# Optimization experiments

Measured on AMD Instinct MI355X. Metric: run time of the kernel, lower is better.

## Reference

```python
import jax, jax.numpy as jnp
import numpy as np

HEADS = 16
HEAD_DIM = 64
QUAD_C = 5.0   # 2quad: exp(x) ~ (x + c)^2
EPS = 1e-6


def setup_inputs() -> dict:
    key = jax.random.key(0)
    k1, k2, k3 = jax.random.split(key, 3)
    B, T, H = 2, 2048, 1024
    x = jax.random.normal(k1, (B, T, H), dtype=jnp.float32)
    # scaled init to keep pre-activation scores sane
    Wqkv = jax.random.normal(k2, (H, 3 * H), dtype=jnp.float32) * (H ** -0.5)
    Wo = jax.random.normal(k3, (H, H), dtype=jnp.float32) * (H ** -0.5)
    tau = jnp.full((HEADS,), 5.0, dtype=jnp.float32)
    return {"x": x, "Wqkv": Wqkv, "Wo": Wo, "tau": tau}


def reference(x, Wqkv, Wo, tau):
    B, T, C = x.shape
    h, d = HEADS, HEAD_DIM
    qkv = x @ Wqkv                                  # [B,T,3C]
    q, k, v = jnp.split(qkv, 3, axis=-1)
    q = q.reshape(B, T, h, d).transpose(0, 2, 1, 3)  # [B,h,T,d]
    k = k.reshape(B, T, h, d).transpose(0, 2, 1, 3)
    v = v.reshape(B, T, h, d).transpose(0, 2, 1, 3)
    # tau-scaled scores
    s = jnp.einsum("bhqd,bhkd->bhqk", q, k) / (jnp.sqrt(jnp.float32(d)) * tau[None, :, None, None])
    # 2quad attention: (s + c)^2 normalized over keys (non-softmax)
    e = jnp.square(s + QUAD_C)                       # [B,h,T,T], >=0
    w = e / (jnp.sum(e, axis=-1, keepdims=True) + EPS)
    out = jnp.einsum("bhqk,bhkd->bhqd", w, v)        # [B,h,T,d]
    out = out.transpose(0, 2, 1, 3).reshape(B, T, C)
    return out @ Wo
```

## Files before the change

kernel.cpp:

```cpp
#include <hip/hip_runtime.h>
#include <hip/hip_bf16.h>


typedef unsigned short ushort_t;
typedef __attribute__((ext_vector_type(8))) short short8;
typedef __attribute__((ext_vector_type(4))) float f32x4;
typedef __attribute__((ext_vector_type(16))) float f32x16;

#define B_      2
#define T_      2048
#define C_      1024
#define HEADS_  16
#define D_      64

union frag_u { unsigned u[4]; short8 s8; };

__device__ __forceinline__ ushort_t f2bf(float f) {
  __hip_bfloat16 h = __float2bfloat16(f);
  return *reinterpret_cast<ushort_t*>(&h);
}

__device__ __forceinline__ unsigned cvt_pk_bf16(float lo, float hi) {
  unsigned r;
  asm("v_cvt_pk_bf16_f32 %0, %1, %2" : "=v"(r) : "v"(lo), "v"(hi));
  return r;
}

__device__ __forceinline__ void permlane32_swap(unsigned &a, unsigned &b) {
  asm volatile("v_permlane32_swap_b32 %0, %1" : "+v"(a), "+v"(b));
}

__device__ __forceinline__ f32x16 zero16() {
  f32x16 z;
#pragma unroll
  for (int i = 0; i < 16; ++i) z[i] = 0.f;
  return z;
}

__global__ __launch_bounds__(256) void cast_x_kernel(const float* __restrict__ x,
                                                     ushort_t* __restrict__ xb) {
  int i = blockIdx.x * 256 + threadIdx.x;
  float4 f = ((const float4*)x)[i];
  ushort_t* o = xb + (size_t)i * 4;
  o[0] = f2bf(f.x); o[1] = f2bf(f.y); o[2] = f2bf(f.z); o[3] = f2bf(f.w);
}

__global__ __launch_bounds__(256) void transpose_cast_w(const float* __restrict__ in,
                                                        ushort_t* __restrict__ out,
                                                        int R, int Cc) {
  __shared__ float tile[64][65];
  int rb = blockIdx.y, cb = blockIdx.x;
  int c = threadIdx.x & 63;
  int r0 = threadIdx.x >> 6;
#pragma unroll
  for (int i = 0; i < 16; ++i) {
    int r = r0 + i * 4;
    tile[r][c] = in[(size_t)(rb * 64 + r) * Cc + cb * 64 + c];
  }
  __syncthreads();
#pragma unroll
  for (int i = 0; i < 16; ++i) {
    int r = r0 + i * 4;
    out[(size_t)(cb * 64 + r) * R + rb * 64 + c] = f2bf(tile[c][r]);
  }
}

__global__ __launch_bounds__(256) void transpose_v_kernel(const ushort_t* __restrict__ v,
                                                          ushort_t* __restrict__ vT) {
  __shared__ ushort_t tile[64][72];
  int bh = blockIdx.y, tb = blockIdx.x;
  int c = threadIdx.x & 63;
  int r0 = threadIdx.x >> 6;
#pragma unroll
  for (int i = 0; i < 16; ++i) {
    int r = r0 + i * 4;
    tile[r][c] = v[((size_t)bh * T_ + tb * 64 + r) * D_ + c];
  }
  __syncthreads();
#pragma unroll
  for (int i = 0; i < 16; ++i) {
    int r = r0 + i * 4;
    vT[((size_t)bh * D_ + r) * T_ + tb * 64 + c] = tile[c][r];
  }
}

__device__ __forceinline__ void gemm_tile(const ushort_t* __restrict__ A,
                                          const ushort_t* __restrict__ Bt,
                                          int K, int tm, int tn,
                                          ushort_t* lds, f32x4 acc[4][4]) {
  const int tid = threadIdx.x;
  const int lane = tid & 63, wave = tid >> 6;
  const int wm = wave >> 1, wn = wave & 1;
  const int lr = lane & 15, lk = lane >> 4;
  ushort_t* As = lds;
  ushort_t* Bs = lds + 128 * 72;
  const ushort_t* Ag = A + (size_t)tm * 128 * K;
  const ushort_t* Bg = Bt + (size_t)tn * 128 * K;

  for (int kt = 0; kt < K; kt += 64) {
#pragma unroll
    for (int i = 0; i < 4; ++i) {
      int cch = tid + i * 256; int row = cch >> 3, kc = cch & 7;
      *(short8*)&As[row * 72 + kc * 8] =
          *(const short8*)&Ag[(size_t)row * K + kt + kc * 8];
    }
#pragma unroll
    for (int i = 0; i < 4; ++i) {
      int cch = tid + i * 256; int row = cch >> 3, kc = cch & 7;
      *(short8*)&Bs[row * 72 + kc * 8] =
          *(const short8*)&Bg[(size_t)row * K + kt + kc * 8];
    }
    __syncthreads();
#pragma unroll
    for (int kk = 0; kk < 64; kk += 32) {
      short8 a[4], b[4];
#pragma unroll
      for (int m = 0; m < 4; ++m)
        a[m] = *(const short8*)&As[(wm * 64 + m * 16 + lr) * 72 + kk + lk * 8];
#pragma unroll
      for (int n = 0; n < 4; ++n)
        b[n] = *(const short8*)&Bs[(wn * 64 + n * 16 + lr) * 72 + kk + lk * 8];
#pragma unroll
      for (int m = 0; m < 4; ++m)
#pragma unroll
        for (int n = 0; n < 4; ++n)
          acc[m][n] = __builtin_amdgcn_mfma_f32_16x16x32_bf16(a[m], b[n], acc[m][n], 0, 0, 0);
    }
    __syncthreads();
  }
}

__global__ __launch_bounds__(256) void gemm_qkv(const ushort_t* __restrict__ xb,
                                                const ushort_t* __restrict__ wT,
                                                ushort_t* __restrict__ qg,
                                                ushort_t* __restrict__ kg,
                                                ushort_t* __restrict__ vg) {
  __shared__ __align__(16) ushort_t lds[2 * 128 * 72];
  f32x4 acc[4][4];
#pragma unroll
  for (int m = 0; m < 4; ++m)
#pragma unroll
    for (int n = 0; n < 4; ++n) acc[m][n] = (f32x4){0.f, 0.f, 0.f, 0.f};

  gemm_tile(xb, wT, C_, blockIdx.y, blockIdx.x, lds, acc);

  const int lane = threadIdx.x & 63, wave = threadIdx.x >> 6;
  const int wm = wave >> 1, wn = wave & 1;
  const int lr = lane & 15, lk = lane >> 4;
#pragma unroll
  for (int m = 0; m < 4; ++m)
#pragma unroll
    for (int n = 0; n < 4; ++n)
#pragma unroll
      for (int r = 0; r < 4; ++r) {
        int row = blockIdx.y * 128 + wm * 64 + m * 16 + lk * 4 + r;
        int col = blockIdx.x * 128 + wn * 64 + n * 16 + lr;
        int b = row >> 11, t = row & 2047;
        int part = col >> 10, idx = col & 1023;
        int h = idx >> 6, j = idx & 63;
        ushort_t* dst = (part == 0) ? qg : (part == 1) ? kg : vg;
        dst[(((size_t)(b * HEADS_ + h)) * T_ + t) * D_ + j] = f2bf(acc[m][n][r]);
      }
}

__global__ __launch_bounds__(256) void gemm_out(const ushort_t* __restrict__ ab,
                                                const ushort_t* __restrict__ woT,
                                                float* __restrict__ out) {
  __shared__ __align__(16) ushort_t lds[2 * 128 * 72];
  f32x4 acc[4][4];
#pragma unroll
  for (int m = 0; m < 4; ++m)
#pragma unroll
    for (int n = 0; n < 4; ++n) acc[m][n] = (f32x4){0.f, 0.f, 0.f, 0.f};

  gemm_tile(ab, woT, C_, blockIdx.y, blockIdx.x, lds, acc);

  const int lane = threadIdx.x & 63, wave = threadIdx.x >> 6;
  const int wm = wave >> 1, wn = wave & 1;
  const int lr = lane & 15, lk = lane >> 4;
#pragma unroll
  for (int m = 0; m < 4; ++m)
#pragma unroll
    for (int n = 0; n < 4; ++n)
#pragma unroll
      for (int r = 0; r < 4; ++r) {
        int row = blockIdx.y * 128 + wm * 64 + m * 16 + lk * 4 + r;
        int col = blockIdx.x * 128 + wn * 64 + n * 16 + lr;
        out[(size_t)row * C_ + col] = acc[m][n][r];
      }
}

__global__ __launch_bounds__(256, 2) void attn_kernel(const ushort_t* __restrict__ qg,
                                                      const ushort_t* __restrict__ kg,
                                                      const ushort_t* __restrict__ vTg,
                                                      const float* __restrict__ tau,
                                                      ushort_t* __restrict__ attn_out) {
  __shared__ __align__(16) ushort_t kvbuf[128 * 72 + 64 * 136];
  __shared__ float denom_lds[2][2][2][32];
  ushort_t* Ks  = kvbuf;
  ushort_t* Vts = kvbuf + 128 * 72;

  const int tid = threadIdx.x, lane = tid & 63;
  const int w = tid >> 6, wq = w >> 1, wk = w & 1;
  const int l31 = lane & 31, hi = lane >> 5, hi8 = hi * 8;
  const int qt = blockIdx.x, bh = blockIdx.y;
  const int b = bh >> 4, h = bh & 15;
  const float inv = 1.0f / (8.0f * tau[h]);

  const ushort_t* kb_ = kg  + (size_t)bh * T_ * D_;
  const ushort_t* vb_ = vTg + (size_t)bh * D_ * T_;
  const ushort_t* qp  = qg  + ((size_t)bh * T_ + qt * 128 + wq * 64) * D_;

  const int krow[4] = { (tid) >> 3, (tid + 256) >> 3, (tid + 512) >> 3, (tid + 768) >> 3 };
  const int kcol = (tid & 7) * 8;
  const int vrow[4] = { (tid) >> 4, (tid + 256) >> 4, (tid + 512) >> 4, (tid + 768) >> 4 };
  const int vcol = (tid & 15) * 8;

  short8 qf[2][4];
#pragma unroll
  for (int qb = 0; qb < 2; ++qb)
#pragma unroll
    for (int dc = 0; dc < 4; ++dc)
      qf[qb][dc] = *(const short8*)&qp[(qb * 32 + l31) * D_ + dc * 16 + hi8];

  f32x16 acc[2][2];
  acc[0][0] = zero16(); acc[0][1] = zero16();
  acc[1][0] = zero16(); acc[1][1] = zero16();
  float denomp[2] = {0.f, 0.f};

  short8 kreg[4], vreg[4];
#pragma unroll
  for (int i = 0; i < 4; ++i) {
    kreg[i] = *(const short8*)&kb_[(size_t)krow[i] * D_ + kcol];
    vreg[i] = *(const short8*)&vb_[(size_t)vrow[i] * T_ + vcol];
  }

  const int NT = T_ / 128;
  for (int rnd = 0; rnd < NT; ++rnd) {
#pragma unroll
    for (int i = 0; i < 4; ++i) {
      *(short8*)&Ks[krow[i] * 72 + kcol] = kreg[i];
      *(short8*)&Vts[vrow[i] * 136 + vcol] = vreg[i];
    }
    __syncthreads();

    if (rnd + 1 < NT) {
      const int kv0 = (rnd + 1) * 128;
#pragma unroll
      for (int i = 0; i < 4; ++i) {
        kreg[i] = *(const short8*)&kb_[(size_t)(kv0 + krow[i]) * D_ + kcol];
        vreg[i] = *(const short8*)&vb_[(size_t)vrow[i] * T_ + kv0 + vcol];
      }
    }

#pragma unroll
    for (int kb = 0; kb < 2; ++kb) {
      const int krow0 = wk * 64 + kb * 32;
      f32x16 s[2]; s[0] = zero16(); s[1] = zero16();
#pragma unroll
      for (int dc = 0; dc < 4; ++dc) {
        short8 kf = *(const short8*)&Ks[(krow0 + l31) * 72 + dc * 16 + hi8];
        s[0] = __builtin_amdgcn_mfma_f32_32x32x16_bf16(kf, qf[0][dc], s[0], 0, 0, 0);
        s[1] = __builtin_amdgcn_mfma_f32_32x32x16_bf16(kf, qf[1][dc], s[1], 0, 0, 0);
      }

      frag_u ef[2][2];
#pragma unroll
      for (int qb = 0; qb < 2; ++qb) {
        float ev[16];
        float dsum = 0.f;
#pragma unroll
        for (int r = 0; r < 16; ++r) {
          float t = fmaf(s[qb][r], inv, 5.0f);
          ev[r] = t * t;
          dsum += ev[r];
        }
        denomp[qb] += dsum;
        unsigned P[8];
#pragma unroll
        for (int p = 0; p < 8; ++p) P[p] = cvt_pk_bf16(ev[2 * p], ev[2 * p + 1]);
        unsigned a0 = P[0], b0 = P[2]; permlane32_swap(a0, b0);
        unsigned a1 = P[1], b1 = P[3]; permlane32_swap(a1, b1);
        ef[qb][0].u[0] = a0; ef[qb][0].u[1] = a1; ef[qb][0].u[2] = b0; ef[qb][0].u[3] = b1;
        unsigned a2 = P[4], b2 = P[6]; permlane32_swap(a2, b2);
        unsigned a3 = P[5], b3 = P[7]; permlane32_swap(a3, b3);
        ef[qb][1].u[0] = a2; ef[qb][1].u[1] = a3; ef[qb][1].u[2] = b2; ef[qb][1].u[3] = b3;
      }

#pragma unroll
      for (int c = 0; c < 2; ++c)
#pragma unroll
        for (int db = 0; db < 2; ++db) {
          short8 vf = *(const short8*)&Vts[(db * 32 + l31) * 136 + krow0 + c * 16 + hi8];
          acc[0][db] = __builtin_amdgcn_mfma_f32_32x32x16_bf16(ef[0][c].s8, vf, acc[0][db], 0, 0, 0);
          acc[1][db] = __builtin_amdgcn_mfma_f32_32x32x16_bf16(ef[1][c].s8, vf, acc[1][db], 0, 0, 0);
        }
    }
    __syncthreads();
  }

#pragma unroll
  for (int qb = 0; qb < 2; ++qb) {
    float v = denomp[qb];
    v += __shfl_xor(v, 32);
    if (lane < 32) denom_lds[wk][wq][qb][l31] = v;
  }
  float* out_lds = (float*)kvbuf;
  if (wk == 1) {
#pragma unroll
    for (int qb = 0; qb < 2; ++qb)
#pragma unroll
      for (int db = 0; db < 2; ++db)
#pragma unroll
        for (int r = 0; r < 16; ++r) {
          int qr = qb * 32 + (r & 3) + 8 * (r >> 2) + 4 * hi;
          out_lds[(wq * 64 + qr) * 64 + db * 32 + l31] = acc[qb][db][r];
        }
  }
  __syncthreads();
  if (wk == 0) {
#pragma unroll
    for (int qb = 0; qb < 2; ++qb)
#pragma unroll
      for (int r = 0; r < 16; ++r) {
        int cr = (r & 3) + 8 * (r >> 2) + 4 * hi;
        int qr = qb * 32 + cr;
        float dt = denom_lds[0][wq][qb][cr] + denom_lds[1][wq][qb][cr];
        float dinv = 1.0f / (dt + 1e-6f);
#pragma unroll
        for (int db = 0; db < 2; ++db) {
          float val = acc[qb][db][r] + out_lds[(wq * 64 + qr) * 64 + db * 32 + l31];
          int grow = b * T_ + qt * 128 + wq * 64 + qr;
          attn_out[(size_t)grow * C_ + h * 64 + db * 32 + l31] = f2bf(val * dinv);
        }
      }
  }
}

extern "C" void kernel_launch(void* const* d_in, const int* in_sizes, int n_in,
                              void* d_out, int out_size, void* d_ws, size_t ws_size,
                              hipStream_t stream) {
  const float* x    = (const float*)d_in[0];
  const float* Wqkv = (const float*)d_in[1];
  const float* Wo   = (const float*)d_in[2];
  const float* tau  = (const float*)d_in[3];
  float* out = (float*)d_out;

  char* ws = (char*)d_ws;
  ushort_t* xb    = (ushort_t*)(ws);
  ushort_t* wqkvT = (ushort_t*)(ws + 8388608);
  ushort_t* woT   = (ushort_t*)(ws + 14680064);
  ushort_t* qg    = (ushort_t*)(ws + 16777216);
  ushort_t* kg    = (ushort_t*)(ws + 25165824);
  ushort_t* ab    = (ushort_t*)(ws + 33554432);
  ushort_t* vg  = (ushort_t*)d_out;
  ushort_t* vTg = (ushort_t*)d_out + 4194304;

  cast_x_kernel<<<4096, 256, 0, stream>>>(x, xb);
  transpose_cast_w<<<dim3(48, 16), 256, 0, stream>>>(Wqkv, wqkvT, 1024, 3072);
  transpose_cast_w<<<dim3(16, 16), 256, 0, stream>>>(Wo, woT, 1024, 1024);
  gemm_qkv<<<dim3(24, 32), 256, 0, stream>>>(xb, wqkvT, qg, kg, vg);
  transpose_v_kernel<<<dim3(32, 32), 256, 0, stream>>>(vg, vTg);
  attn_kernel<<<dim3(16, 32), 256, 0, stream>>>(qg, kg, vTg, tau, ab);
  gemm_out<<<dim3(8, 32), 256, 0, stream>>>(ab, woT, out);
}
```

Baseline: 127.3 us.

## Split attention key dimension across two blocks and add a combine kernel

Splits the key/value sequence of the attention kernel into two halves on a third grid dimension, so twice as many blocks run with half the loop each. Each half writes unnormalized fp16 partial numerators and fp32 partial denominators, and a new combine kernel sums them, normalizes, and writes the bf16 attention output. The aim is better occupancy and GPU fill, since the original grid had only 512 blocks. In exchange it adds an extra launch, extra global traffic for the partials, and fp16 rounding of the partial sums. Workspace regions are reused as aliases to hold vT and the partials.

Measured after the change: 135.4 us. 1.06x slower.

```diff
diff --git a/kernel.cpp b/kernel.cpp
--- a/kernel.cpp
+++ b/kernel.cpp
@@ -4,6 +4,7 @@
 
 typedef unsigned short ushort_t;
 typedef __attribute__((ext_vector_type(8))) short short8;
+typedef __attribute__((ext_vector_type(8))) _Float16 half8;
 typedef __attribute__((ext_vector_type(4))) float f32x4;
 typedef __attribute__((ext_vector_type(16))) float f32x16;
 
@@ -194,7 +195,8 @@
                                                       const ushort_t* __restrict__ kg,
                                                       const ushort_t* __restrict__ vTg,
                                                       const float* __restrict__ tau,
-                                                      ushort_t* __restrict__ attn_out) {
+                                                      _Float16* __restrict__ numerP,
+                                                      float* __restrict__ denomP) {
   __shared__ __align__(16) ushort_t kvbuf[128 * 72 + 64 * 136];
   __shared__ float denom_lds[2][2][2][32];
   ushort_t* Ks  = kvbuf;
@@ -203,12 +205,12 @@
   const int tid = threadIdx.x, lane = tid & 63;
   const int w = tid >> 6, wq = w >> 1, wk = w & 1;
   const int l31 = lane & 31, hi = lane >> 5, hi8 = hi * 8;
-  const int qt = blockIdx.x, bh = blockIdx.y;
-  const int b = bh >> 4, h = bh & 15;
+  const int qt = blockIdx.x, bh = blockIdx.y, z = blockIdx.z;
+  const int h = bh & 15;
   const float inv = 1.0f / (8.0f * tau[h]);
 
-  const ushort_t* kb_ = kg  + (size_t)bh * T_ * D_;
-  const ushort_t* vb_ = vTg + (size_t)bh * D_ * T_;
+  const ushort_t* kb_ = kg  + (size_t)bh * T_ * D_ + (size_t)z * 1024 * D_;
+  const ushort_t* vb_ = vTg + (size_t)bh * D_ * T_ + (size_t)z * 1024;
   const ushort_t* qp  = qg  + ((size_t)bh * T_ + qt * 128 + wq * 64) * D_;
 
   const int krow[4] = { (tid) >> 3, (tid + 256) >> 3, (tid + 512) >> 3, (tid + 768) >> 3 };
@@ -235,7 +237,7 @@
     vreg[i] = *(const short8*)&vb_[(size_t)vrow[i] * T_ + vcol];
   }
 
-  const int NT = T_ / 128;
+  const int NT = 1024 / 128;
   for (int rnd = 0; rnd < NT; ++rnd) {
 #pragma unroll
     for (int i = 0; i < 4; ++i) {
@@ -318,23 +320,49 @@
         }
   }
   __syncthreads();
+  const size_t qbase = ((size_t)z * 32 + bh) * T_ + qt * 128 + wq * 64;
   if (wk == 0) {
+    if (lane < 32) {
+#pragma unroll
+      for (int qb = 0; qb < 2; ++qb) {
+        float dt = denom_lds[0][wq][qb][l31] + denom_lds[1][wq][qb][l31];
+        denomP[qbase + qb * 32 + l31] = dt;
+      }
+    }
 #pragma unroll
     for (int qb = 0; qb < 2; ++qb)
 #pragma unroll
       for (int r = 0; r < 16; ++r) {
         int cr = (r & 3) + 8 * (r >> 2) + 4 * hi;
         int qr = qb * 32 + cr;
-        float dt = denom_lds[0][wq][qb][cr] + denom_lds[1][wq][qb][cr];
-        float dinv = 1.0f / (dt + 1e-6f);
 #pragma unroll
         for (int db = 0; db < 2; ++db) {
           float val = acc[qb][db][r] + out_lds[(wq * 64 + qr) * 64 + db * 32 + l31];
-          int grow = b * T_ + qt * 128 + wq * 64 + qr;
-          attn_out[(size_t)grow * C_ + h * 64 + db * 32 + l31] = f2bf(val * dinv);
+          numerP[(qbase + qr) * D_ + db * 32 + l31] = (_Float16)val;
         }
       }
   }
+}
+
+__global__ __launch_bounds__(256) void combine_kernel(const _Float16* __restrict__ numerP,
+                                                      const float* __restrict__ denomP,
+                                                      ushort_t* __restrict__ ab) {
+  int gid = blockIdx.x * 256 + threadIdx.x;
+  int dg = gid & 7;
+  int q = (gid >> 3) & 2047;
+  int bh = gid >> 14;
+  size_t nidx = (((size_t)bh) * T_ + q) * D_ + dg * 8;
+  const size_t halfN = (size_t)32 * T_ * D_;
+  half8 n0 = *(const half8*)&numerP[nidx];
+  half8 n1 = *(const half8*)&numerP[halfN + nidx];
+  float dt = denomP[(size_t)bh * T_ + q] + denomP[(size_t)32 * T_ + bh * T_ + q] + 1e-6f;
+  float dinv = 1.0f / dt;
+  int b = bh >> 4, h = bh & 15;
+  ushort_t tmp[8];
+#pragma unroll
+  for (int i = 0; i < 8; ++i)
+    tmp[i] = f2bf(((float)n0[i] + (float)n1[i]) * dinv);
+  *(short8*)&ab[((size_t)(b * T_) + q) * C_ + h * 64 + dg * 8] = *(short8*)tmp;
 }
 
 extern "C" void kernel_launch(void* const* d_in, const int* in_sizes, int n_in,
@@ -348,19 +376,22 @@
 
   char* ws = (char*)d_ws;
   ushort_t* xb    = (ushort_t*)(ws);
+  ushort_t* vTg   = (ushort_t*)(ws);
   ushort_t* wqkvT = (ushort_t*)(ws + 8388608);
+  float*    denomP= (float*)   (ws + 8388608);
   ushort_t* woT   = (ushort_t*)(ws + 14680064);
   ushort_t* qg    = (ushort_t*)(ws + 16777216);
   ushort_t* kg    = (ushort_t*)(ws + 25165824);
   ushort_t* ab    = (ushort_t*)(ws + 33554432);
-  ushort_t* vg  = (ushort_t*)d_out;
-  ushort_t* vTg = (ushort_t*)d_out + 4194304;
+  ushort_t* vg     = (ushort_t*)d_out;
+  _Float16* numerP = (_Float16*)d_out;
 
   cast_x_kernel<<<4096, 256, 0, stream>>>(x, xb);
   transpose_cast_w<<<dim3(48, 16), 256, 0, stream>>>(Wqkv, wqkvT, 1024, 3072);
   transpose_cast_w<<<dim3(16, 16), 256, 0, stream>>>(Wo, woT, 1024, 1024);
   gemm_qkv<<<dim3(24, 32), 256, 0, stream>>>(xb, wqkvT, qg, kg, vg);
   transpose_v_kernel<<<dim3(32, 32), 256, 0, stream>>>(vg, vTg);
-  attn_kernel<<<dim3(16, 32), 256, 0, stream>>>(qg, kg, vTg, tau, ab);
+  attn_kernel<<<dim3(16, 32, 2), 256, 0, stream>>>(qg, kg, vTg, tau, numerP, denomP);
+  combine_kernel<<<2048, 256, 0, stream>>>(numerP, denomP, ab);
   gemm_out<<<dim3(8, 32), 256, 0, stream>>>(ab, woT, out);
 }
```
